# Optimization experiments

Hardware: AMD Instinct MI355X
Metric: run time of the kernel (lower is better)

The kernel has to match this reference:

```python
import jax, jax.numpy as jnp
import numpy as np

D_K = 64  # hardcoded in source module

def setup_inputs() -> dict:
    key = jax.random.key(0)
    kq, kk, kv, km = jax.random.split(key, 4)
    B, H, S, D = 2, 16, 2048, D_K
    Q = jax.random.normal(kq, (B, H, S, D), dtype=jnp.float32)
    K = jax.random.normal(kk, (B, H, S, D), dtype=jnp.float32)
    V = jax.random.normal(kv, (B, H, S, D), dtype=jnp.float32)
    # boolean mask: True positions are masked out (filled with -1e9)
    attn_mask = jax.random.randint(km, (B, H, S, S), 0, 2) == 1
    return {"Q": Q, "K": K, "V": V, "attn_mask": attn_mask}

def reference(Q, K, V, attn_mask):
    scale = 1.0 / np.sqrt(D_K).astype(np.float32)
    # scores: [B, H, S, S]
    scores = jnp.einsum('bhqd,bhkd->bhqk', Q, K) * scale
    scores = jnp.where(attn_mask, jnp.float32(-1e9), scores)
    attn = jax.nn.softmax(scores, axis=-1)
    context = jnp.einsum('bhqk,bhkd->bhqd', attn, V)
    return context
```

## Files before the change

kernel.cpp:

```cpp
#include <hip/hip_runtime.h>

#define SEQ   2048
#define DK    64
#define QBLK  64
#define KVBLK 64
#define NTILE (SEQ / KVBLK)
#define PITCH 72

typedef __attribute__((ext_vector_type(8))) __bf16 bf16x8;
typedef __attribute__((ext_vector_type(4))) __bf16 bf16x4;
typedef __attribute__((ext_vector_type(2))) __bf16 bf16x2;
typedef __attribute__((ext_vector_type(4))) float  f32x4;
typedef __attribute__((ext_vector_type(4))) int    i32x4;

template<int CTRL>
__device__ __forceinline__ float dpp_ror(float v) {
  int i = __builtin_bit_cast(int, v);
  int r = __builtin_amdgcn_update_dpp(i, i, CTRL, 0xf, 0xf, false);
  return __builtin_bit_cast(float, r);
}
__device__ __forceinline__ float grp16_max(float v) {
  v = fmaxf(v, dpp_ror<0x128>(v));
  v = fmaxf(v, dpp_ror<0x124>(v));
  v = fmaxf(v, dpp_ror<0x122>(v));
  v = fmaxf(v, dpp_ror<0x121>(v));
  return v;
}
__device__ __forceinline__ float grp16_sum(float v) {
  v += dpp_ror<0x128>(v);
  v += dpp_ror<0x124>(v);
  v += dpp_ror<0x122>(v);
  v += dpp_ror<0x121>(v);
  return v;
}

__device__ __forceinline__ void block_sync_lds() {
  asm volatile("s_waitcnt lgkmcnt(0)" ::: "memory");
  __builtin_amdgcn_sched_barrier(0);
  __builtin_amdgcn_s_barrier();
  __builtin_amdgcn_sched_barrier(0);
}

__global__ __launch_bounds__(256, 2)
void sdpa_fwd(const float* __restrict__ Q, const float* __restrict__ K,
              const float* __restrict__ V, const int* __restrict__ M,
              float* __restrict__ O)
{
  __shared__ __bf16 Klds[KVBLK][PITCH];
  __shared__ __bf16 Vt[DK][PITCH];
  __shared__ __bf16 Plds[4][16][PITCH];

  const int tid  = threadIdx.x;
  const int w    = tid >> 6;
  const int lane = tid & 63;
  const int g    = lane >> 4;
  const int li   = lane & 15;

  const int bid = blockIdx.x;
  const int blk = (bid & 7) * 128 + (bid >> 3);
  const int qb  = blk & (SEQ / QBLK - 1);
  const int bh  = blk >> 5;

  const float* Qp = Q + (size_t)bh * SEQ * DK;
  const float* Kp = K + (size_t)bh * SEQ * DK;
  const float* Vp = V + (size_t)bh * SEQ * DK;
  const int*   Mp = M + (size_t)bh * SEQ * SEQ;
  float*       Op = O + (size_t)bh * SEQ * DK;

  const int q0 = qb * QBLK + w * 16;

  const int sk = tid >> 2;
  const int sd = (tid & 3) * 16;
  const int sj = ((sk & 3) << 4) | (sk >> 2);
  const int vk = (tid & 31) * 2;
  const int vd = (tid >> 5) * 8;

  bf16x8 qfrag[2];
  {
    const float qs = 0.125f * 1.44269504088896340736f;
    const float* qr = Qp + (size_t)(q0 + li) * DK + g * 8;
    #pragma unroll
    for (int h2 = 0; h2 < 2; ++h2) {
      f32x4 a = *(const f32x4*)(qr + h2 * 32);
      f32x4 b = *(const f32x4*)(qr + h2 * 32 + 4);
      bf16x8 f;
      #pragma unroll
      for (int e = 0; e < 4; ++e) { f[e] = (__bf16)(a[e] * qs); f[4 + e] = (__bf16)(b[e] * qs); }
      qfrag[h2] = f;
    }
  }

  f32x4 acc[4];
  #pragma unroll
  for (int c = 0; c < 4; ++c) acc[c] = (f32x4){0.f, 0.f, 0.f, 0.f};
  float m_r[4], l_r[4];
  #pragma unroll
  for (int r = 0; r < 4; ++r) { m_r[r] = -__builtin_inff(); l_r[r] = 0.f; }

  f32x4 kA[4], vA[4];
  i32x4 mA[4];

  {
    const float* ks  = Kp + (size_t)sk * DK + sd;
    const float* vs0 = Vp + (size_t)vk * DK + vd;
    const float* vs1 = Vp + (size_t)(vk + 1) * DK + vd;
    #pragma unroll
    for (int i = 0; i < 4; ++i) kA[i] = *(const f32x4*)(ks + 4 * i);
    vA[0] = *(const f32x4*)vs0; vA[1] = *(const f32x4*)(vs0 + 4);
    vA[2] = *(const f32x4*)vs1; vA[3] = *(const f32x4*)(vs1 + 4);
    #pragma unroll
    for (int r = 0; r < 4; ++r)
      mA[r] = *(const i32x4*)(Mp + (size_t)(q0 + 4 * g + r) * SEQ + li * 4);
  }

  for (int kt = 0; kt < NTILE; ++kt) {
    block_sync_lds();

    {
      bf16x8 klo, khi;
      #pragma unroll
      for (int e = 0; e < 4; ++e) {
        klo[e] = (__bf16)kA[0][e]; klo[4 + e] = (__bf16)kA[1][e];
        khi[e] = (__bf16)kA[2][e]; khi[4 + e] = (__bf16)kA[3][e];
      }
      *(bf16x8*)&Klds[sj][sd]     = klo;
      *(bf16x8*)&Klds[sj][sd + 8] = khi;
      #pragma unroll
      for (int j = 0; j < 4; ++j) {
        bf16x2 p0; p0[0] = (__bf16)vA[0][j]; p0[1] = (__bf16)vA[2][j];
        bf16x2 p1; p1[0] = (__bf16)vA[1][j]; p1[1] = (__bf16)vA[3][j];
        *(bf16x2*)&Vt[vd + j][vk]     = p0;
        *(bf16x2*)&Vt[vd + 4 + j][vk] = p1;
      }
    }

    i32x4 msk[4];
    #pragma unroll
    for (int r = 0; r < 4; ++r) msk[r] = mA[r];
    {
      const int tn = (kt + 1 < NTILE) ? kt + 1 : 0;
      #pragma unroll
      for (int r = 0; r < 4; ++r)
        mA[r] = *(const i32x4*)(Mp + (size_t)(q0 + 4 * g + r) * SEQ + tn * KVBLK + li * 4);
      const float* ks  = Kp + (size_t)(tn * KVBLK + sk) * DK + sd;
      const float* vs0 = Vp + (size_t)(tn * KVBLK + vk) * DK + vd;
      const float* vs1 = Vp + (size_t)(tn * KVBLK + vk + 1) * DK + vd;
      #pragma unroll
      for (int i = 0; i < 4; ++i) kA[i] = *(const f32x4*)(ks + 4 * i);
      vA[0] = *(const f32x4*)vs0; vA[1] = *(const f32x4*)(vs0 + 4);
      vA[2] = *(const f32x4*)vs1; vA[3] = *(const f32x4*)(vs1 + 4);
    }

    block_sync_lds();

    f32x4 st[4];
    #pragma unroll
    for (int nt = 0; nt < 4; ++nt) {
      bf16x8 b0 = *(const bf16x8*)&Klds[nt * 16 + li][g * 8];
      bf16x8 b1 = *(const bf16x8*)&Klds[nt * 16 + li][32 + g * 8];
      f32x4 s = (f32x4){0.f, 0.f, 0.f, 0.f};
      s = __builtin_amdgcn_mfma_f32_16x16x32_bf16(qfrag[0], b0, s, 0, 0, 0);
      s = __builtin_amdgcn_mfma_f32_16x16x32_bf16(qfrag[1], b1, s, 0, 0, 0);
      st[nt] = s;
    }

    #pragma unroll
    for (int r = 0; r < 4; ++r) {
      float s0 = msk[r].x ? -1e9f : st[0][r];
      float s1 = msk[r].y ? -1e9f : st[1][r];
      float s2 = msk[r].z ? -1e9f : st[2][r];
      float s3 = msk[r].w ? -1e9f : st[3][r];
      float mx    = grp16_max(fmaxf(fmaxf(s0, s1), fmaxf(s2, s3)));
      float mnew  = fmaxf(m_r[r], mx);
      float alpha = __builtin_amdgcn_exp2f(m_r[r] - mnew);
      float p0 = __builtin_amdgcn_exp2f(s0 - mnew);
      float p1 = __builtin_amdgcn_exp2f(s1 - mnew);
      float p2 = __builtin_amdgcn_exp2f(s2 - mnew);
      float p3 = __builtin_amdgcn_exp2f(s3 - mnew);
      l_r[r] = l_r[r] * alpha + grp16_sum((p0 + p1) + (p2 + p3));
      m_r[r] = mnew;
      acc[0][r] *= alpha;
      acc[1][r] *= alpha;
      acc[2][r] *= alpha;
      acc[3][r] *= alpha;
      bf16x4 pk;
      pk[0] = (__bf16)p0; pk[1] = (__bf16)p1; pk[2] = (__bf16)p2; pk[3] = (__bf16)p3;
      *(bf16x4*)&Plds[w][4 * g + r][li * 4] = pk;
    }

    asm volatile("s_waitcnt lgkmcnt(0)" ::: "memory");
    __builtin_amdgcn_sched_barrier(0);

    bf16x8 pa0 = *(const bf16x8*)&Plds[w][li][g * 8];
    bf16x8 pa1 = *(const bf16x8*)&Plds[w][li][32 + g * 8];
    #pragma unroll
    for (int dt = 0; dt < 4; ++dt) {
      bf16x8 v0 = *(const bf16x8*)&Vt[dt * 16 + li][g * 8];
      bf16x8 v1 = *(const bf16x8*)&Vt[dt * 16 + li][32 + g * 8];
      acc[dt] = __builtin_amdgcn_mfma_f32_16x16x32_bf16(pa0, v0, acc[dt], 0, 0, 0);
      acc[dt] = __builtin_amdgcn_mfma_f32_16x16x32_bf16(pa1, v1, acc[dt], 0, 0, 0);
    }
  }

  #pragma unroll
  for (int r = 0; r < 4; ++r) {
    float inv = 1.0f / l_r[r];
    float* orow = Op + (size_t)(q0 + 4 * g + r) * DK + li;
    #pragma unroll
    for (int dt = 0; dt < 4; ++dt)
      orow[dt * 16] = acc[dt][r] * inv;
  }
}

extern "C" void kernel_launch(void* const* d_in, const int* in_sizes, int n_in,
                              void* d_out, int out_size, void* d_ws, size_t ws_size,
                              hipStream_t stream) {
  const float* Q = (const float*)d_in[0];
  const float* K = (const float*)d_in[1];
  const float* V = (const float*)d_in[2];
  const int*   M = (const int*)d_in[3];
  float*       O = (float*)d_out;

  const int nblocks = 2 * 16 * (SEQ / QBLK);
  sdpa_fwd<<<nblocks, 256, 0, stream>>>(Q, K, V, M, O);
}
```

Measured before the change: 761.2 us.

## Double query rows per block to reuse K/V tiles across two Q fragments

```diff
diff --git a/kernel.cpp b/kernel.cpp
--- a/kernel.cpp
+++ b/kernel.cpp
@@ -1,11 +1,12 @@
 #include <hip/hip_runtime.h>
 
-#define SEQ   2048
-#define DK    64
-#define QBLK  64
-#define KVBLK 64
-#define NTILE (SEQ / KVBLK)
-#define PITCH 72
+#define SEQ    2048
+#define DK     64
+#define QBLK   128
+#define KVBLK  64
+#define NTILE  (SEQ / KVBLK)
+#define PITCH  72
+#define PPITCH 72
 
 typedef __attribute__((ext_vector_type(8))) __bf16 bf16x8;
 typedef __attribute__((ext_vector_type(4))) __bf16 bf16x4;
@@ -48,7 +49,7 @@
 {
   __shared__ __bf16 Klds[KVBLK][PITCH];
   __shared__ __bf16 Vt[DK][PITCH];
-  __shared__ __bf16 Plds[4][16][PITCH];
+  __shared__ __bf16 Plds[4][32][PPITCH];
 
   const int tid  = threadIdx.x;
   const int w    = tid >> 6;
@@ -57,9 +58,9 @@
   const int li   = lane & 15;
 
   const int bid = blockIdx.x;
-  const int blk = (bid & 7) * 128 + (bid >> 3);
+  const int blk = (bid & 7) * 64 + (bid >> 3);
   const int qb  = blk & (SEQ / QBLK - 1);
-  const int bh  = blk >> 5;
+  const int bh  = blk >> 4;
 
   const float* Qp = Q + (size_t)bh * SEQ * DK;
   const float* Kp = K + (size_t)bh * SEQ * DK;
@@ -75,10 +76,11 @@
   const int vk = (tid & 31) * 2;
   const int vd = (tid >> 5) * 8;
 
-  bf16x8 qfrag[2];
-  {
+  bf16x8 qfrag[2][2];
+  #pragma unroll
+  for (int m = 0; m < 2; ++m) {
     const float qs = 0.125f * 1.44269504088896340736f;
-    const float* qr = Qp + (size_t)(q0 + li) * DK + g * 8;
+    const float* qr = Qp + (size_t)(q0 + m * 64 + li) * DK + g * 8;
     #pragma unroll
     for (int h2 = 0; h2 < 2; ++h2) {
       f32x4 a = *(const f32x4*)(qr + h2 * 32);
@@ -86,19 +88,23 @@
       bf16x8 f;
       #pragma unroll
       for (int e = 0; e < 4; ++e) { f[e] = (__bf16)(a[e] * qs); f[4 + e] = (__bf16)(b[e] * qs); }
-      qfrag[h2] = f;
+      qfrag[m][h2] = f;
     }
   }
 
-  f32x4 acc[4];
-  #pragma unroll
-  for (int c = 0; c < 4; ++c) acc[c] = (f32x4){0.f, 0.f, 0.f, 0.f};
-  float m_r[4], l_r[4];
-  #pragma unroll
-  for (int r = 0; r < 4; ++r) { m_r[r] = -__builtin_inff(); l_r[r] = 0.f; }
+  f32x4 acc[2][4];
+  #pragma unroll
+  for (int m = 0; m < 2; ++m)
+    #pragma unroll
+    for (int c = 0; c < 4; ++c) acc[m][c] = (f32x4){0.f, 0.f, 0.f, 0.f};
+  float m_r[2][4], l_r[2][4];
+  #pragma unroll
+  for (int m = 0; m < 2; ++m)
+    #pragma unroll
+    for (int r = 0; r < 4; ++r) { m_r[m][r] = -__builtin_inff(); l_r[m][r] = 0.f; }
 
   f32x4 kA[4], vA[4];
-  i32x4 mA[4];
+  i32x4 mA[8];
 
   {
     const float* ks  = Kp + (size_t)sk * DK + sd;
@@ -109,8 +115,11 @@
     vA[0] = *(const f32x4*)vs0; vA[1] = *(const f32x4*)(vs0 + 4);
     vA[2] = *(const f32x4*)vs1; vA[3] = *(const f32x4*)(vs1 + 4);
     #pragma unroll
-    for (int r = 0; r < 4; ++r)
-      mA[r] = *(const i32x4*)(Mp + (size_t)(q0 + 4 * g + r) * SEQ + li * 4);
+    for (int m = 0; m < 2; ++m)
+      #pragma unroll
+      for (int r = 0; r < 4; ++r)
+        mA[m * 4 + r] = __builtin_nontemporal_load(
+            (const i32x4*)(Mp + (size_t)(q0 + m * 64 + 4 * g + r) * SEQ + li * 4));
   }
 
   for (int kt = 0; kt < NTILE; ++kt) {
@@ -134,14 +143,9 @@
       }
     }
 
-    i32x4 msk[4];
-    #pragma unroll
-    for (int r = 0; r < 4; ++r) msk[r] = mA[r];
+    const int tn = (kt + 1 < NTILE) ? kt + 1 : 0;
+
     {
-      const int tn = (kt + 1 < NTILE) ? kt + 1 : 0;
-      #pragma unroll
-      for (int r = 0; r < 4; ++r)
-        mA[r] = *(const i32x4*)(Mp + (size_t)(q0 + 4 * g + r) * SEQ + tn * KVBLK + li * 4);
       const float* ks  = Kp + (size_t)(tn * KVBLK + sk) * DK + sd;
       const float* vs0 = Vp + (size_t)(tn * KVBLK + vk) * DK + vd;
       const float* vs1 = Vp + (size_t)(tn * KVBLK + vk + 1) * DK + vd;
@@ -153,63 +157,74 @@
 
     block_sync_lds();
 
-    f32x4 st[4];
-    #pragma unroll
-    for (int nt = 0; nt < 4; ++nt) {
-      bf16x8 b0 = *(const bf16x8*)&Klds[nt * 16 + li][g * 8];
-      bf16x8 b1 = *(const bf16x8*)&Klds[nt * 16 + li][32 + g * 8];
-      f32x4 s = (f32x4){0.f, 0.f, 0.f, 0.f};
-      s = __builtin_amdgcn_mfma_f32_16x16x32_bf16(qfrag[0], b0, s, 0, 0, 0);
-      s = __builtin_amdgcn_mfma_f32_16x16x32_bf16(qfrag[1], b1, s, 0, 0, 0);
-      st[nt] = s;
-    }
-
-    #pragma unroll
-    for (int r = 0; r < 4; ++r) {
-      float s0 = msk[r].x ? -1e9f : st[0][r];
-      float s1 = msk[r].y ? -1e9f : st[1][r];
-      float s2 = msk[r].z ? -1e9f : st[2][r];
-      float s3 = msk[r].w ? -1e9f : st[3][r];
-      float mx    = grp16_max(fmaxf(fmaxf(s0, s1), fmaxf(s2, s3)));
-      float mnew  = fmaxf(m_r[r], mx);
-      float alpha = __builtin_amdgcn_exp2f(m_r[r] - mnew);
-      float p0 = __builtin_amdgcn_exp2f(s0 - mnew);
-      float p1 = __builtin_amdgcn_exp2f(s1 - mnew);
-      float p2 = __builtin_amdgcn_exp2f(s2 - mnew);
-      float p3 = __builtin_amdgcn_exp2f(s3 - mnew);
-      l_r[r] = l_r[r] * alpha + grp16_sum((p0 + p1) + (p2 + p3));
-      m_r[r] = mnew;
-      acc[0][r] *= alpha;
-      acc[1][r] *= alpha;
-      acc[2][r] *= alpha;
-      acc[3][r] *= alpha;
-      bf16x4 pk;
-      pk[0] = (__bf16)p0; pk[1] = (__bf16)p1; pk[2] = (__bf16)p2; pk[3] = (__bf16)p3;
-      *(bf16x4*)&Plds[w][4 * g + r][li * 4] = pk;
+    #pragma unroll
+    for (int m = 0; m < 2; ++m) {
+      f32x4 st[4];
+      #pragma unroll
+      for (int nt = 0; nt < 4; ++nt) {
+        bf16x8 b0 = *(const bf16x8*)&Klds[nt * 16 + li][g * 8];
+        bf16x8 b1 = *(const bf16x8*)&Klds[nt * 16 + li][32 + g * 8];
+        f32x4 s = (f32x4){0.f, 0.f, 0.f, 0.f};
+        s = __builtin_amdgcn_mfma_f32_16x16x32_bf16(qfrag[m][0], b0, s, 0, 0, 0);
+        s = __builtin_amdgcn_mfma_f32_16x16x32_bf16(qfrag[m][1], b1, s, 0, 0, 0);
+        st[nt] = s;
+      }
+
+      #pragma unroll
+      for (int r = 0; r < 4; ++r) {
+        i32x4 mm = mA[m * 4 + r];
+        mA[m * 4 + r] = __builtin_nontemporal_load(
+            (const i32x4*)(Mp + (size_t)(q0 + m * 64 + 4 * g + r) * SEQ + tn * KVBLK + li * 4));
+        float s0 = mm.x ? -1e9f : st[0][r];
+        float s1 = mm.y ? -1e9f : st[1][r];
+        float s2 = mm.z ? -1e9f : st[2][r];
+        float s3 = mm.w ? -1e9f : st[3][r];
+        float mx    = grp16_max(fmaxf(fmaxf(s0, s1), fmaxf(s2, s3)));
+        float mnew  = fmaxf(m_r[m][r], mx);
+        float alpha = __builtin_amdgcn_exp2f(m_r[m][r] - mnew);
+        float p0 = __builtin_amdgcn_exp2f(s0 - mnew);
+        float p1 = __builtin_amdgcn_exp2f(s1 - mnew);
+        float p2 = __builtin_amdgcn_exp2f(s2 - mnew);
+        float p3 = __builtin_amdgcn_exp2f(s3 - mnew);
+        l_r[m][r] = l_r[m][r] * alpha + grp16_sum((p0 + p1) + (p2 + p3));
+        m_r[m][r] = mnew;
+        acc[m][0][r] *= alpha;
+        acc[m][1][r] *= alpha;
+        acc[m][2][r] *= alpha;
+        acc[m][3][r] *= alpha;
+        bf16x4 pk;
+        pk[0] = (__bf16)p0; pk[1] = (__bf16)p1; pk[2] = (__bf16)p2; pk[3] = (__bf16)p3;
+        *(bf16x4*)&Plds[w][m * 16 + 4 * g + r][li * 4] = pk;
+      }
     }
 
     asm volatile("s_waitcnt lgkmcnt(0)" ::: "memory");
     __builtin_amdgcn_sched_barrier(0);
 
-    bf16x8 pa0 = *(const bf16x8*)&Plds[w][li][g * 8];
-    bf16x8 pa1 = *(const bf16x8*)&Plds[w][li][32 + g * 8];
     #pragma unroll
     for (int dt = 0; dt < 4; ++dt) {
       bf16x8 v0 = *(const bf16x8*)&Vt[dt * 16 + li][g * 8];
       bf16x8 v1 = *(const bf16x8*)&Vt[dt * 16 + li][32 + g * 8];
-      acc[dt] = __builtin_amdgcn_mfma_f32_16x16x32_bf16(pa0, v0, acc[dt], 0, 0, 0);
-      acc[dt] = __builtin_amdgcn_mfma_f32_16x16x32_bf16(pa1, v1, acc[dt], 0, 0, 0);
+      #pragma unroll
+      for (int m = 0; m < 2; ++m) {
+        bf16x8 pa0 = *(const bf16x8*)&Plds[w][m * 16 + li][g * 8];
+        bf16x8 pa1 = *(const bf16x8*)&Plds[w][m * 16 + li][32 + g * 8];
+        acc[m][dt] = __builtin_amdgcn_mfma_f32_16x16x32_bf16(pa0, v0, acc[m][dt], 0, 0, 0);
+        acc[m][dt] = __builtin_amdgcn_mfma_f32_16x16x32_bf16(pa1, v1, acc[m][dt], 0, 0, 0);
+      }
     }
   }
 
   #pragma unroll
-  for (int r = 0; r < 4; ++r) {
-    float inv = 1.0f / l_r[r];
-    float* orow = Op + (size_t)(q0 + 4 * g + r) * DK + li;
-    #pragma unroll
-    for (int dt = 0; dt < 4; ++dt)
-      orow[dt * 16] = acc[dt][r] * inv;
-  }
+  for (int m = 0; m < 2; ++m)
+    #pragma unroll
+    for (int r = 0; r < 4; ++r) {
+      float inv = 1.0f / l_r[m][r];
+      float* orow = Op + (size_t)(q0 + m * 64 + 4 * g + r) * DK + li;
+      #pragma unroll
+      for (int dt = 0; dt < 4; ++dt)
+        __builtin_nontemporal_store(acc[m][dt][r] * inv, &orow[dt * 16]);
+    }
 }
 
 extern "C" void kernel_launch(void* const* d_in, const int* in_sizes, int n_in,
```

Result: faster. 725.0 us (-4.8%).
